# Kernel optimization log

Measured on AMD Instinct MI355X. Metric: run time of the kernel, lower is better.

The kernel has to match this reference:

```python
import jax, jax.numpy as jnp
import numpy as np

A = 22          # players per frame (11 home + 11 away)
F_IN = 16       # in_channels
HEADS = 4       # gnn_head
C = 128         # gnn_hidden_dim
HID = 256       # lstm_hidden_dim
B, T = 32, 256


def gat_layer(x, W, att_src, att_dst, bias, concat):
    """PyG GATConv on a complete graph with self-loops (dense per-frame attention).
    x: [N, A, Fin]; W: [Fin, H*C]; att_src/att_dst: [H, C]; bias: [H*C] or [C].
    edge_attr is ignored (edge_dim=None in the original constructor)."""
    H = att_src.shape[0]
    N, A_, Fin = x.shape
    h = jnp.einsum('naf,fhc->nahc', x, W.reshape(Fin, H, -1))   # [N,A,H,C]
    a_src = jnp.sum(h * att_src, axis=-1)                        # [N,A,H]
    a_dst = jnp.sum(h * att_dst, axis=-1)                        # [N,A,H]
    e = a_dst[:, :, None, :] + a_src[:, None, :, :]              # [N,i,j,H]
    e = jax.nn.leaky_relu(e, 0.2)
    alpha = jax.nn.softmax(e, axis=2)                            # softmax over sources j
    out = jnp.einsum('nijh,njhc->nihc', alpha, h)                # [N,A,H,C]
    out = out.reshape(N, A_, -1) if concat else out.mean(axis=2)
    return out + bias


def lstm_layer(x, mask, Wih, Whh, bih, bhh):
    """Masked LSTM layer == pack_padded_sequence semantics (state frozen past seq_len).
    x: [B,T,in], mask: [B,T] bool. Returns (outputs [B,T,H], h_last [B,H])."""
    Bb, Tt, _ = x.shape
    H = Whh.shape[1]
    xT = jnp.swapaxes(x, 0, 1)                   # [T,B,in]
    mT = jnp.swapaxes(mask, 0, 1)[..., None]     # [T,B,1]
    h0 = jnp.zeros((Bb, H), x.dtype)
    c0 = jnp.zeros((Bb, H), x.dtype)

    def step(carry, inp):
        h, c = carry
        xt, mt = inp
        g = xt @ Wih.T + h @ Whh.T + bih + bhh
        i, f, gg, o = jnp.split(g, 4, axis=-1)   # torch gate order i,f,g,o
        i = jax.nn.sigmoid(i)
        f = jax.nn.sigmoid(f)
        gg = jnp.tanh(gg)
        o = jax.nn.sigmoid(o)
        c_new = f * c + i * gg
        h_new = o * jnp.tanh(c_new)
        h = jnp.where(mt, h_new, h)
        c = jnp.where(mt, c_new, c)
        return (h, c), h

    (h_last, _), hs = jax.lax.scan(step, (h0, c0), (xT, mT))
    return jnp.swapaxes(hs, 0, 1), h_last


def setup_inputs() -> dict:
    key = jax.random.key(0)
    ks = jax.random.split(key, 24)
    rn = lambda k, shape, fan: jax.random.normal(k, shape, jnp.float32) / np.sqrt(fan)
    inp = {
        'features': jax.random.normal(ks[0], (B, T, A, F_IN), jnp.float32),
        'seq_lengths': jax.random.randint(ks[1], (B,), T // 2, T + 1).astype(jnp.int64),
        # GAT layer 1: in=16 -> heads=4, C=128, concat
        'W1': rn(ks[2], (F_IN, HEADS * C), F_IN),
        'att_src1': rn(ks[3], (HEADS, C), C),
        'att_dst1': rn(ks[4], (HEADS, C), C),
        'b1': jnp.zeros((HEADS * C,), jnp.float32),
        # GAT layer 2: in=512 -> heads=1, C=128, avg
        'W2': rn(ks[5], (HEADS * C, C), HEADS * C),
        'att_src2': rn(ks[6], (1, C), C),
        'att_dst2': rn(ks[7], (1, C), C),
        'b2': jnp.zeros((C,), jnp.float32),
        # LSTM layer 0 (input 128 -> 256) and layer 1 (256 -> 256)
        'Wih0': rn(ks[8], (4 * HID, C), C),
        'Whh0': rn(ks[9], (4 * HID, HID), HID),
        'bih0': jnp.zeros((4 * HID,), jnp.float32),
        'bhh0': jnp.zeros((4 * HID,), jnp.float32),
        'Wih1': rn(ks[10], (4 * HID, HID), HID),
        'Whh1': rn(ks[11], (4 * HID, HID), HID),
        'bih1': jnp.zeros((4 * HID,), jnp.float32),
        'bhh1': jnp.zeros((4 * HID,), jnp.float32),
        # classifier
        'clf_w': rn(ks[12], (1, HID), HID),
        'clf_b': jnp.zeros((1,), jnp.float32),
    }
    return inp


def reference(features, seq_lengths, W1, att_src1, att_dst1, b1,
              W2, att_src2, att_dst2, b2,
              Wih0, Whh0, bih0, bhh0, Wih1, Whh1, bih1, bhh1,
              clf_w, clf_b):
    Bb, Tt, A_, Fin = features.shape
    mask = jnp.arange(Tt)[None, :] < seq_lengths[:, None]          # [B,T]
    x = features.reshape(Bb * Tt, A_, Fin)                          # all frames, vectorized
    x = jax.nn.relu(gat_layer(x, W1, att_src1, att_dst1, b1, True))
    x = jax.nn.relu(gat_layer(x, W2, att_src2, att_dst2, b2, False))
    pooled = x.mean(axis=1).reshape(Bb, Tt, -1)                     # global_mean_pool per frame
    pooled = jnp.where(mask[..., None], pooled, 0.0)                # invalid frames -> 0
    h1, _ = lstm_layer(pooled, mask, Wih0, Whh0, bih0, bhh0)
    _, h_last = lstm_layer(h1, mask, Wih1, Whh1, bih1, bhh1)        # h_n[-1]
    logits = (h_last @ clf_w.T + clf_b).squeeze(-1)                 # [B]
    return logits
```

## Files before the change

### kernel.cpp

```cpp
#include <hip/hip_runtime.h>
#include <math.h>

#define A_PL 22
#define F_IN_ 16
#define T_LEN 256
#define NBLK_SEQ 64

typedef unsigned long long ull;

__device__ __forceinline__ float sigmoidf_(float x) { return 1.f / (1.f + __expf(-x)); }

__device__ __forceinline__ void gstore(float* p, float v) {
  __hip_atomic_store(p, v, __ATOMIC_RELAXED, __HIP_MEMORY_SCOPE_AGENT);
}
__device__ __forceinline__ float gload(const float* p) {
  return __hip_atomic_load(p, __ATOMIC_RELAXED, __HIP_MEMORY_SCOPE_AGENT);
}

__device__ __forceinline__ void dwait(unsigned* arr, int tlo, int thi) {
  if (threadIdx.x < 64) {
    const int lane = threadIdx.x;
    int t = (lane < 32) ? tlo : thi;
    if (t < 0) t = 0;
    const unsigned tu = (unsigned)t;
    while (__hip_atomic_load(arr + lane * 32, __ATOMIC_ACQUIRE,
                             __HIP_MEMORY_SCOPE_AGENT) < tu) {
      __builtin_amdgcn_s_sleep(1);
    }
  }
  __syncthreads();
  __builtin_amdgcn_fence(__ATOMIC_ACQUIRE, "agent");
}

__device__ __forceinline__ float dpp_xor1(float v) {
  int r = __builtin_amdgcn_mov_dpp(__builtin_bit_cast(int, v), 0xB1, 0xF, 0xF, true);
  return __builtin_bit_cast(float, r);
}
__device__ __forceinline__ float dpp_xor2(float v) {
  int r = __builtin_amdgcn_mov_dpp(__builtin_bit_cast(int, v), 0x4E, 0xF, 0xF, true);
  return __builtin_bit_cast(float, r);
}

__device__ __forceinline__ int read_len(const int* __restrict__ lens, int b) {
  return (lens[1] == 0) ? lens[2 * b] : lens[b];
}

__global__ __launch_bounds__(256) void gat_naive(
    const float* __restrict__ feat, const int* __restrict__ lens,
    const float* __restrict__ W1, const float* __restrict__ as1,
    const float* __restrict__ ad1, const float* __restrict__ b1,
    const float* __restrict__ W2, const float* __restrict__ as2,
    const float* __restrict__ ad2, const float* __restrict__ b2,
    float* __restrict__ xT)
{
  const int n = blockIdx.x;
  const int tid = threadIdx.x;
  const int bb = n >> 8;
  const int tt = n & 255;
  if (tt >= read_len(lens, bb)) {
    if (tid < 128) xT[((size_t)tt * 128 + tid) * 32 + bb] = 0.f;
    return;
  }

  __shared__ float xs[352];
  __shared__ float hbuf[2816];
  __shared__ float x2s[11264];
  __shared__ float asrc[22], adst[22], alpha[484];

  for (int i = tid; i < 352; i += 256) xs[i] = feat[(size_t)n * 352 + i];
  __syncthreads();

  const int c_ = tid & 127;
  const int ap_ = tid >> 7;

  for (int hd = 0; hd < 4; hd++) {
    {
      float wreg[16];
      #pragma unroll
      for (int f = 0; f < 16; f++) wreg[f] = W1[f * 512 + hd * 128 + c_];
      #pragma unroll
      for (int q = 0; q < 11; q++) {
        const int a = ap_ + 2 * q;
        float acc = 0.f;
        #pragma unroll
        for (int f4 = 0; f4 < 4; f4++) {
          const float4 x4 = *(const float4*)(xs + a * 16 + f4 * 4);
          acc += x4.x * wreg[f4 * 4] + x4.y * wreg[f4 * 4 + 1]
               + x4.z * wreg[f4 * 4 + 2] + x4.w * wreg[f4 * 4 + 3];
        }
        hbuf[a * 128 + c_] = acc;
      }
    }
    __syncthreads();
    if (tid < 44) {
      int a = tid >> 1;
      const float* av = (tid & 1) ? ad1 : as1;
      float s = 0.f;
      for (int c = 0; c < 128; c++) s += hbuf[a * 128 + c] * av[hd * 128 + c];
      ((tid & 1) ? adst : asrc)[a] = s;
    }
    __syncthreads();
    if (tid < 22) {
      float ev[22], m = -1e30f;
      for (int j = 0; j < 22; j++) {
        float e = adst[tid] + asrc[j];
        e = (e > 0.f) ? e : 0.2f * e;
        ev[j] = e; if (e > m) m = e;
      }
      float s = 0.f;
      for (int j = 0; j < 22; j++) { ev[j] = __expf(ev[j] - m); s += ev[j]; }
      float inv = 1.f / s;
      for (int j = 0; j < 22; j++) alpha[tid * 22 + j] = ev[j] * inv;
    }
    __syncthreads();
    for (int i = tid; i < 2816; i += 256) {
      int a = i >> 7, c = i & 127;
      float acc = 0.f;
      for (int j = 0; j < 22; j++) acc += alpha[a * 22 + j] * hbuf[j * 128 + c];
      x2s[a * 512 + hd * 128 + c] = fmaxf(acc + b1[hd * 128 + c], 0.f);
    }
    __syncthreads();
  }

  {
    float acc[11];
    #pragma unroll
    for (int q = 0; q < 11; q++) acc[q] = 0.f;
    for (int k = 0; k < 512; k += 4) {
      const float w0 = W2[(size_t)(k + 0) * 128 + c_];
      const float w1 = W2[(size_t)(k + 1) * 128 + c_];
      const float w2 = W2[(size_t)(k + 2) * 128 + c_];
      const float w3 = W2[(size_t)(k + 3) * 128 + c_];
      #pragma unroll
      for (int q = 0; q < 11; q++) {
        const float4 x4 = *(const float4*)(x2s + (ap_ + 2 * q) * 512 + k);
        acc[q] += x4.x * w0 + x4.y * w1 + x4.z * w2 + x4.w * w3;
      }
    }
    #pragma unroll
    for (int q = 0; q < 11; q++) hbuf[(ap_ + 2 * q) * 128 + c_] = acc[q];
  }
  __syncthreads();
  if (tid < 44) {
    int a = tid >> 1;
    const float* av = (tid & 1) ? ad2 : as2;
    float s = 0.f;
    for (int c = 0; c < 128; c++) s += hbuf[a * 128 + c] * av[c];
    ((tid & 1) ? adst : asrc)[a] = s;
  }
  __syncthreads();
  if (tid < 22) {
    float ev[22], m = -1e30f;
    for (int j = 0; j < 22; j++) {
      float e = adst[tid] + asrc[j];
      e = (e > 0.f) ? e : 0.2f * e;
      ev[j] = e; if (e > m) m = e;
    }
    float s = 0.f;
    for (int j = 0; j < 22; j++) { ev[j] = __expf(ev[j] - m); s += ev[j]; }
    float inv = 1.f / s;
    for (int j = 0; j < 22; j++) alpha[tid * 22 + j] = ev[j] * inv;
  }
  __syncthreads();
  if (tid < 128) {
    float s = 0.f;
    for (int a = 0; a < 22; a++) {
      float v = b2[tid];
      for (int j = 0; j < 22; j++) v += alpha[a * 22 + j] * hbuf[j * 128 + tid];
      s += fmaxf(v, 0.f);
    }
    xT[((size_t)tt * 128 + tid) * 32 + bb] = s * (1.f / 22.f);
  }
}

template<int KK>
__device__ __forceinline__ void lstm_body(
    const int j0, const float* __restrict__ xT,
    const float* __restrict__ Wih, const float* __restrict__ Whh,
    const float* __restrict__ bih, const float* __restrict__ bhh,
    const int* __restrict__ lens,
    float* __restrict__ h0T, float* __restrict__ h1T,
    unsigned* __restrict__ arr, const int bid,
    float* __restrict__ hs, float* __restrict__ gates)
{
  constexpr int NK = KK / 16;
  constexpr bool IS1 = (KK == 512);
  const int tid = threadIdx.x;
  const int kp = tid & 15;
  const int cg = (tid >> 4) & 7;
  const int bg = tid >> 7;
  const int c0 = cg * 4;
  const int b0 = bg * 8;
  const int sw = (kp & 7) << 2;
  const float* hpA = hs + kp * 32 + (b0 ^ sw);
  const float* hpB = hs + kp * 32 + ((b0 + 4) ^ sw);

  float wr[4][NK];
  {
    const int r0 = ((c0 >> 3) << 8) + j0 + (c0 & 7);
    #pragma unroll
    for (int ci = 0; ci < 4; ci++) {
      const int r = r0 + ci;
      #pragma unroll
      for (int t = 0; t < NK; t++) {
        const int k = kp + 16 * t;
        if (IS1) wr[ci][t] = (k < 256) ? Wih[r * 256 + k] : Whh[r * 256 + k - 256];
        else     wr[ci][t] = (k < 128) ? Wih[r * 128 + k] : Whh[r * 256 + k - 128];
      }
    }
  }

  const int nb = tid >> 3, njl = tid & 7;
  float bb0 = 0.f, bb1 = 0.f, bb2 = 0.f, bb3 = 0.f;
  int len_b = T_LEN;
  if (tid < 256) {
    const int j = j0 + njl;
    bb0 = bih[j]       + bhh[j];
    bb1 = bih[256 + j] + bhh[256 + j];
    bb2 = bih[512 + j] + bhh[512 + j];
    bb3 = bih[768 + j] + bhh[768 + j];
    len_b = read_len(lens, nb);
  }
  float creg = 0.f;

  const int PMAX = IS1 ? T_LEN : (T_LEN - 1);
  for (int p = 0; p <= PMAX; p++) {
    if (p > 0) dwait(arr, p, IS1 ? p : p - 2);
    const bool compute = IS1 ? (p >= 1) : true;

    if (compute) {
      if (IS1) {
        const float* s0 = h0T + (size_t)((p - 1) & 3) * 8192;
        const float* s1 = h1T + (size_t)((p + 2) & 3) * 8192;
        #pragma unroll
        for (int i = tid; i < 4096; i += 512) {
          const int k = i >> 3, b4 = (i & 7) << 2;
          const float4 v = (k < 256)
              ? *(const float4*)(s0 + (k << 5) + b4)
              : *(const float4*)(s1 + ((k - 256) << 5) + b4);
          *(float4*)(hs + (k << 5) + (b4 ^ ((k & 7) << 2))) = v;
        }
      } else {
        const float* xp = xT + (size_t)p * 4096;
        const float* s0 = h0T + (size_t)((p + 3) & 3) * 8192;
        #pragma unroll
        for (int i = tid; i < 3072; i += 512) {
          const int k = i >> 3, b4 = (i & 7) << 2;
          const float4 v = (k < 128)
              ? *(const float4*)(xp + (k << 5) + b4)
              : *(const float4*)(s0 + ((k - 128) << 5) + b4);
          *(float4*)(hs + (k << 5) + (b4 ^ ((k & 7) << 2))) = v;
        }
      }
      __syncthreads();

      float a[4][8] = {};
      #pragma unroll
      for (int t = 0; t < NK; t++) {
        const float4 hA = *(const float4*)(hpA + t * 512);
        const float4 hB = *(const float4*)(hpB + t * 512);
        #pragma unroll
        for (int ci = 0; ci < 4; ci++) {
          const float w = wr[ci][t];
          a[ci][0] += w * hA.x; a[ci][1] += w * hA.y;
          a[ci][2] += w * hA.z; a[ci][3] += w * hA.w;
          a[ci][4] += w * hB.x; a[ci][5] += w * hB.y;
          a[ci][6] += w * hB.z; a[ci][7] += w * hB.w;
        }
      }
      #pragma unroll
      for (int ci = 0; ci < 4; ci++) {
        #pragma unroll
        for (int bi = 0; bi < 8; bi++) {
          float v = a[ci][bi];
          v += dpp_xor1(v);
          v += dpp_xor2(v);
          v += __shfl_xor(v, 4);
          v += __shfl_xor(v, 8);
          a[ci][bi] = v;
        }
      }
      float g0 = 0.f, g1 = 0.f;
      #pragma unroll
      for (int ci = 0; ci < 4; ci++) {
        #pragma unroll
        for (int bq = 0; bq < 4; bq++) {
          if ((kp & 3) == ci && (kp >> 2) == bq) { g0 = a[ci][bq]; g1 = a[ci][bq + 4]; }
        }
      }
      gates[(b0 + (kp >> 2)) * 34 + c0 + (kp & 3)] = g0;
      gates[(b0 + 4 + (kp >> 2)) * 34 + c0 + (kp & 3)] = g1;
      __syncthreads();

      if (tid < 256) {
        const float gi = gates[nb * 34 + njl];
        const float gf = gates[nb * 34 + 8 + njl];
        const float gg = gates[nb * 34 + 16 + njl];
        const float go = gates[nb * 34 + 24 + njl];
        const float iv = sigmoidf_(gi + bb0);
        const float fv = sigmoidf_(gf + bb1);
        const float gv = tanhf(gg + bb2);
        const float ov = sigmoidf_(go + bb3);
        const float cnew = fv * creg + iv * gv;
        const float hnew = ov * tanhf(cnew);
        const int t_eff = IS1 ? (p - 1) : p;
        const bool valid = t_eff < len_b;
        const int kold = (IS1 ? 256 : 128) + j0 + njl;
        const float hold = hs[(kold << 5) + (nb ^ ((kold & 7) << 2))];
        const float houtv = valid ? hnew : hold;
        if (valid) creg = cnew;
        float* dst = (IS1 ? h1T + (size_t)((p + 3) & 3) * 8192
                          : h0T + (size_t)(p & 3) * 8192)
                     + (j0 + njl) * 32 + nb;
        gstore(dst, houtv);
      }
    }

    __syncthreads();
    if (tid == 0)
      __hip_atomic_store(arr + bid * 32, (unsigned)(p + 1), __ATOMIC_RELEASE,
                         __HIP_MEMORY_SCOPE_AGENT);
  }
}

__global__ __launch_bounds__(512, 2) void lstm_pipe(
    const float* __restrict__ xT,
    const float* __restrict__ Wih0, const float* __restrict__ Whh0,
    const float* __restrict__ bih0, const float* __restrict__ bhh0,
    const float* __restrict__ Wih1, const float* __restrict__ Whh1,
    const float* __restrict__ bih1, const float* __restrict__ bhh1,
    const int* __restrict__ lens,
    const float* __restrict__ clfw, const float* __restrict__ clfb,
    float* __restrict__ ws, float* __restrict__ out)
{
  __shared__ float hs[16384];
  __shared__ float gates[32 * 34 + 2];

  unsigned* arr = (unsigned*)ws;
  float* h0T = ws + 2048;
  float* h1T = ws + 2048 + 32768;

  const int bid = blockIdx.x;
  if (bid >= 32)
    lstm_body<512>((bid - 32) * 8, xT, Wih1, Whh1, bih1, bhh1, lens,
                   h0T, h1T, arr, bid, hs, gates);
  else
    lstm_body<384>(bid * 8, xT, Wih0, Whh0, bih0, bhh0, lens,
                   h0T, h1T, arr, bid, hs, gates);

  if (bid == 0) {
    const int tid = threadIdx.x;
    dwait(arr, 0, T_LEN + 1);
    const float* h1f = h1T + (size_t)3 * 8192;
    if (tid < 256) {
      const int b = tid & 31, jg = tid >> 5;
      float s = 0.f;
      #pragma unroll 8
      for (int jj = 0; jj < 32; jj++) {
        const int j = jg * 32 + jj;
        s += gload(h1f + j * 32 + b) * clfw[j];
      }
      gates[jg * 32 + b] = s;
    }
    __syncthreads();
    if (tid < 32) {
      float s = clfb[0];
      #pragma unroll
      for (int g = 0; g < 8; g++) s += gates[g * 32 + tid];
      out[tid] = s;
    }
  }
}

extern "C" void kernel_launch(void* const* d_in, const int* in_sizes, int n_in,
                              void* d_out, int out_size, void* d_ws, size_t ws_size,
                              hipStream_t stream) {
  (void)in_sizes; (void)n_in; (void)out_size; (void)ws_size;
  const float* feat = (const float*)d_in[0];
  const int*   lens = (const int*)d_in[1];
  const float* W1   = (const float*)d_in[2];
  const float* as1  = (const float*)d_in[3];
  const float* ad1  = (const float*)d_in[4];
  const float* b1   = (const float*)d_in[5];
  const float* W2   = (const float*)d_in[6];
  const float* as2  = (const float*)d_in[7];
  const float* ad2  = (const float*)d_in[8];
  const float* b2   = (const float*)d_in[9];
  const float* Wih0 = (const float*)d_in[10];
  const float* Whh0 = (const float*)d_in[11];
  const float* bih0 = (const float*)d_in[12];
  const float* bhh0 = (const float*)d_in[13];
  const float* Wih1 = (const float*)d_in[14];
  const float* Whh1 = (const float*)d_in[15];
  const float* bih1 = (const float*)d_in[16];
  const float* bhh1 = (const float*)d_in[17];
  const float* clfw = (const float*)d_in[18];
  const float* clfb = (const float*)d_in[19];

  float* ws  = (float*)d_ws;
  float* xT  = ws + 2048 + 65536;
  float* outp = (float*)d_out;

  hipMemsetAsync(d_ws, 0, (2048 + 65536) * sizeof(float), stream);

  gat_naive<<<8192, 256, 0, stream>>>(feat, lens, W1, as1, ad1, b1,
                                      W2, as2, ad2, b2, xT);

  void* args[] = {
    (void*)&xT,
    (void*)&Wih0, (void*)&Whh0, (void*)&bih0, (void*)&bhh0,
    (void*)&Wih1, (void*)&Whh1, (void*)&bih1, (void*)&bhh1,
    (void*)&lens, (void*)&clfw, (void*)&clfb, (void*)&ws, (void*)&outp
  };
  hipLaunchCooperativeKernel((const void*)lstm_pipe, dim3(NBLK_SEQ), dim3(512),
                             args, 0, stream);
}
```

Measured before the change: 3.629 ms.

## Stage LSTM weights in LDS and use DPP row rotates for reduction

Per-thread register arrays of LSTM weight slices are replaced by a 64 KB shared-memory weight tile, loaded once per block and read as float4 alongside the hidden state in the inner product loop. This frees a large block of VGPRs. The 16-lane reduction now uses DPP row_ror 4 and 8 instead of two cross-lane shuffles, which is intended to cut the reduction's latency. The cost is an extra LDS read per k-step on a latency-bound recurrent path. Total LDS per block rises to roughly 130 KB, so the min-blocks launch bound is dropped and only one block fits per CU.

```diff
diff --git a/kernel.cpp b/kernel.cpp
--- a/kernel.cpp
+++ b/kernel.cpp
@@ -5,8 +5,6 @@
 #define F_IN_ 16
 #define T_LEN 256
 #define NBLK_SEQ 64
-
-typedef unsigned long long ull;
 
 __device__ __forceinline__ float sigmoidf_(float x) { return 1.f / (1.f + __expf(-x)); }
 
@@ -38,6 +36,14 @@
 }
 __device__ __forceinline__ float dpp_xor2(float v) {
   int r = __builtin_amdgcn_mov_dpp(__builtin_bit_cast(int, v), 0x4E, 0xF, 0xF, true);
+  return __builtin_bit_cast(float, r);
+}
+__device__ __forceinline__ float dpp_ror4(float v) {
+  int r = __builtin_amdgcn_mov_dpp(__builtin_bit_cast(int, v), 0x124, 0xF, 0xF, true);
+  return __builtin_bit_cast(float, r);
+}
+__device__ __forceinline__ float dpp_ror8(float v) {
+  int r = __builtin_amdgcn_mov_dpp(__builtin_bit_cast(int, v), 0x128, 0xF, 0xF, true);
   return __builtin_bit_cast(float, r);
 }
 
@@ -181,7 +187,7 @@
     const int* __restrict__ lens,
     float* __restrict__ h0T, float* __restrict__ h1T,
     unsigned* __restrict__ arr, const int bid,
-    float* __restrict__ hs, float* __restrict__ gates)
+    float* __restrict__ wlds, float* __restrict__ hs, float* __restrict__ gates)
 {
   constexpr int NK = KK / 16;
   constexpr bool IS1 = (KK == 512);
@@ -194,19 +200,15 @@
   const int sw = (kp & 7) << 2;
   const float* hpA = hs + kp * 32 + (b0 ^ sw);
   const float* hpB = hs + kp * 32 + ((b0 + 4) ^ sw);
-
-  float wr[4][NK];
-  {
-    const int r0 = ((c0 >> 3) << 8) + j0 + (c0 & 7);
-    #pragma unroll
-    for (int ci = 0; ci < 4; ci++) {
-      const int r = r0 + ci;
-      #pragma unroll
-      for (int t = 0; t < NK; t++) {
-        const int k = kp + 16 * t;
-        if (IS1) wr[ci][t] = (k < 256) ? Wih[r * 256 + k] : Whh[r * 256 + k - 256];
-        else     wr[ci][t] = (k < 128) ? Wih[r * 128 + k] : Whh[r * 256 + k - 128];
-      }
+  const float* wp  = wlds + kp * 32 + c0;
+
+  for (int c = 0; c < 32; c++) {
+    const int r = ((c >> 3) << 8) + j0 + (c & 7);
+    for (int k = tid; k < KK; k += 512) {
+      float v;
+      if (IS1) v = (k < 256) ? Wih[r * 256 + k] : Whh[r * 256 + (k - 256)];
+      else     v = (k < 128) ? Wih[r * 128 + k] : Whh[r * 256 + (k - 128)];
+      wlds[k * 32 + c] = v;
     }
   }
 
@@ -259,9 +261,11 @@
       for (int t = 0; t < NK; t++) {
         const float4 hA = *(const float4*)(hpA + t * 512);
         const float4 hB = *(const float4*)(hpB + t * 512);
+        const float4 wv = *(const float4*)(wp + t * 512);
+        const float w4[4] = { wv.x, wv.y, wv.z, wv.w };
         #pragma unroll
         for (int ci = 0; ci < 4; ci++) {
-          const float w = wr[ci][t];
+          const float w = w4[ci];
           a[ci][0] += w * hA.x; a[ci][1] += w * hA.y;
           a[ci][2] += w * hA.z; a[ci][3] += w * hA.w;
           a[ci][4] += w * hB.x; a[ci][5] += w * hB.y;
@@ -275,8 +279,8 @@
           float v = a[ci][bi];
           v += dpp_xor1(v);
           v += dpp_xor2(v);
-          v += __shfl_xor(v, 4);
-          v += __shfl_xor(v, 8);
+          v += dpp_ror4(v);
+          v += dpp_ror8(v);
           a[ci][bi] = v;
         }
       }
@@ -323,7 +327,7 @@
   }
 }
 
-__global__ __launch_bounds__(512, 2) void lstm_pipe(
+__global__ __launch_bounds__(512) void lstm_pipe(
     const float* __restrict__ xT,
     const float* __restrict__ Wih0, const float* __restrict__ Whh0,
     const float* __restrict__ bih0, const float* __restrict__ bhh0,
@@ -333,6 +337,7 @@
     const float* __restrict__ clfw, const float* __restrict__ clfb,
     float* __restrict__ ws, float* __restrict__ out)
 {
+  __shared__ float wlds[16384];
   __shared__ float hs[16384];
   __shared__ float gates[32 * 34 + 2];
 
@@ -343,10 +348,10 @@
   const int bid = blockIdx.x;
   if (bid >= 32)
     lstm_body<512>((bid - 32) * 8, xT, Wih1, Whh1, bih1, bhh1, lens,
-                   h0T, h1T, arr, bid, hs, gates);
+                   h0T, h1T, arr, bid, wlds, hs, gates);
   else
     lstm_body<384>(bid * 8, xT, Wih0, Whh0, bih0, bhh0, lens,
-                   h0T, h1T, arr, bid, hs, gates);
+                   h0T, h1T, arr, bid, wlds, hs, gates);
 
   if (bid == 0) {
     const int tid = threadIdx.x;
```

New measurement: 3.710 ms. 2.2% more time.
